# Optimization experiments

Measured on AMD Instinct MI355X. Metric: run time of the kernel, lower is better.

The kernel has to match this reference:

```python
import jax, jax.numpy as jnp
import numpy as np
import math

DIM = 1024
NUM_HEADS = 16
HEAD_DIM = 64
SEQ_LEN = 2048
ATTN_SCALE = 0.12


def cosine_norm(x, eps=1e-12):
    # unit-normalize along last dim
    return x * jax.lax.rsqrt(jnp.sum(x * x, axis=-1, keepdims=True) + eps)


def rotary_tables(T, head_dim):
    dim_quarter = max(1, head_dim // 4)
    angular_freq = (1.0 / 1024.0) ** jnp.linspace(0.0, 1.0, dim_quarter, dtype=jnp.float32)
    angular_freq = jnp.concatenate([angular_freq, jnp.zeros(dim_quarter, dtype=jnp.float32)])  # [head_dim//2]
    t = jnp.arange(T, dtype=jnp.float32)
    theta = t[:, None] * angular_freq[None, :]  # [T, head_dim//2]
    return jnp.cos(theta), jnp.sin(theta)


def apply_rotary(x_BTHD, cos, sin):
    # cos/sin: [T, head_dim//2] -> broadcast [1, T, 1, head_dim//2]
    c = cos[None, :, None, :]
    s = sin[None, :, None, :]
    x1, x2 = jnp.split(x_BTHD, 2, axis=-1)
    y1 = x1 * c + x2 * s
    y2 = -x1 * s + x2 * c
    return jnp.concatenate([y1, y2], axis=-1)


def setup_inputs() -> dict:
    key = jax.random.key(0)
    ks = jax.random.split(key, 6)
    x = jax.random.normal(ks[0], (1, SEQ_LEN, DIM), dtype=jnp.float32)
    init_std = 0.02
    Wq = jax.random.normal(ks[1], (DIM, NUM_HEADS * HEAD_DIM), dtype=jnp.float32) * init_std
    Wk = jax.random.normal(ks[2], (DIM, NUM_HEADS * HEAD_DIM), dtype=jnp.float32) * init_std
    Wv = jax.random.normal(ks[3], (DIM, NUM_HEADS * HEAD_DIM), dtype=jnp.float32) * init_std
    Wo = jax.random.normal(ks[4], (NUM_HEADS * HEAD_DIM, DIM), dtype=jnp.float32) * init_std
    # Scale param: initialized as ones * (1/sqrt(dim)); use rand around that magnitude
    s_qk = jax.random.uniform(ks[5], (NUM_HEADS, HEAD_DIM), dtype=jnp.float32,
                              minval=0.5, maxval=1.5) * (1.0 / math.sqrt(DIM))
    return {"x": x, "Wq": Wq, "Wk": Wk, "Wv": Wv, "Wo": Wo, "s_qk": s_qk}


def reference(x, Wq, Wk, Wv, Wo, s_qk):
    B, T, _ = x.shape
    # projections
    q = (x @ Wq).reshape(B, T, NUM_HEADS, HEAD_DIM)
    k = (x @ Wk).reshape(B, T, NUM_HEADS, HEAD_DIM)
    v = (x @ Wv).reshape(B, T, NUM_HEADS, HEAD_DIM)
    # effective scale: s * (init/scale) with init=1, scale=1/sqrt(dim)
    s_eff = s_qk * math.sqrt(DIM)  # [H, D]
    q = cosine_norm(q) * s_eff[None, None, :, :]
    k = cosine_norm(k) * s_eff[None, None, :, :]
    cos, sin = rotary_tables(T, HEAD_DIM)
    q = apply_rotary(q, cos, sin)
    k = apply_rotary(k, cos, sin)
    # causal attention with fixed scale 0.12 (block_mask == causal)
    scores = jnp.einsum('bthd,bshd->bhts', q, k) * ATTN_SCALE  # [B,H,T,T]
    causal = jnp.tril(jnp.ones((T, T), dtype=bool))
    scores = jnp.where(causal[None, None, :, :], scores, jnp.float32(-1e30))
    attn = jax.nn.softmax(scores, axis=-1)
    y = jnp.einsum('bhts,bshd->bthd', attn, v)
    y = y.reshape(B, T, NUM_HEADS * HEAD_DIM)
    return y @ Wo
```

## Files before the change

### kernel.cpp

```cpp
#include <hip/hip_runtime.h>

typedef unsigned short u16;
typedef unsigned int u32;
typedef __attribute__((ext_vector_type(8))) short bf16x8;
typedef __attribute__((ext_vector_type(4))) float f32x4;

__device__ __forceinline__ u16 f2bf(float x) {
  unsigned u = __float_as_uint(x);
  u += 0x7fffu + ((u >> 16) & 1u);
  return (u16)(u >> 16);
}
__device__ __forceinline__ float bf2f(u16 z) {
  return __uint_as_float((u32)z << 16);
}

__global__ __launch_bounds__(256) void cast_kernel(const float* __restrict__ in,
                                                   u16* __restrict__ out, int n,
                                                   float2* __restrict__ rtab) {
  int g = blockIdx.x * 256 + threadIdx.x;
  int i = g * 4;
  if (i < n) {
    float4 f = *(const float4*)(in + i);
    ushort4 o;
    o.x = f2bf(f.x); o.y = f2bf(f.y); o.z = f2bf(f.z); o.w = f2bf(f.w);
    *(ushort4*)(out + i) = o;
  }
  if (g < 2048 * 16) {
    int t = g >> 4, ii = g & 15;
    float fr = exp2f(-10.0f * (float)ii / 15.0f);
    float th = (float)t * fr;
    rtab[g] = make_float2(cosf(th), sinf(th));
  }
}

__global__ __launch_bounds__(256) void transcast(const float* __restrict__ W0,
                                                 const float* __restrict__ W1,
                                                 const float* __restrict__ W2,
                                                 const float* __restrict__ W3,
                                                 u16* __restrict__ out) {
  __shared__ alignas(16) u16 ls[64 * 72];
  int z = blockIdx.z;
  const float* W = (z == 0) ? W0 : (z == 1) ? W1 : (z == 2) ? W2 : W3;
  u16* o = out + (size_t)z * (1024u * 1024u);
  int kt = blockIdx.y * 64, nt = blockIdx.x * 64;
  int tid = threadIdx.x;
  int r = tid >> 2, c0 = (tid & 3) * 16;
  const float* src = W + (size_t)(kt + r) * 1024 + nt + c0;
  u16 tmp[16];
#pragma unroll
  for (int c = 0; c < 16; c += 4) {
    float4 f = *(const float4*)(src + c);
    tmp[c + 0] = f2bf(f.x); tmp[c + 1] = f2bf(f.y);
    tmp[c + 2] = f2bf(f.z); tmp[c + 3] = f2bf(f.w);
  }
#pragma unroll
  for (int c = 0; c < 16; ++c) ls[r * 72 + c0 + c] = tmp[c];
  __syncthreads();
#pragma unroll
  for (int pass = 0; pass < 4; ++pass) {
    int n = pass * 16 + (tid >> 4);
    int kk = (tid & 15) * 4;
    ushort4 val;
    val.x = ls[(kk + 0) * 72 + n];
    val.y = ls[(kk + 1) * 72 + n];
    val.z = ls[(kk + 2) * 72 + n];
    val.w = ls[(kk + 3) * 72 + n];
    *(ushort4*)(o + (size_t)(nt + n) * 1024 + kt + kk) = val;
  }
}

#define GLD 40

__global__ __launch_bounds__(256) void gemm_qkv(const u16* __restrict__ A,
                                                const u16* __restrict__ Wt,
                                                u16* __restrict__ qb,
                                                u16* __restrict__ kb,
                                                u16* __restrict__ vt,
                                                const float* __restrict__ s_qk,
                                                const float2* __restrict__ rtab) {
  __shared__ alignas(16) u16 As[128 * GLD];
  __shared__ alignas(16) u16 Bs[128 * GLD];
  int z = blockIdx.z;
  const u16* B = Wt + (size_t)z * (1024u * 1024u);
  int tid = threadIdx.x;
  int bm = blockIdx.y * 128, bn = blockIdx.x * 128;
  int lane = tid & 63, w = tid >> 6;
  int wm = (w >> 1) * 64, wn = (w & 1) * 64;
  int m16 = lane & 15, q = lane >> 4;
  f32x4 acc[4][4] = {};
  int srow = tid >> 1, scol = (tid & 1) * 16;
  const u16* aptr = A + (size_t)(bm + srow) * 1024 + scol;
  const u16* bptr = B + (size_t)(bn + srow) * 1024 + scol;
  uint4 a0 = *(const uint4*)(aptr);
  uint4 a1 = *(const uint4*)(aptr + 8);
  uint4 b0 = *(const uint4*)(bptr);
  uint4 b1 = *(const uint4*)(bptr + 8);
  for (int k0 = 0; k0 < 1024; k0 += 32) {
    __syncthreads();
    *(uint4*)&As[srow * GLD + scol] = a0;
    *(uint4*)&As[srow * GLD + scol + 8] = a1;
    *(uint4*)&Bs[srow * GLD + scol] = b0;
    *(uint4*)&Bs[srow * GLD + scol + 8] = b1;
    uint4 na0, na1, nb0, nb1;
    if (k0 < 992) {
      na0 = *(const uint4*)(aptr + k0 + 32);
      na1 = *(const uint4*)(aptr + k0 + 40);
      nb0 = *(const uint4*)(bptr + k0 + 32);
      nb1 = *(const uint4*)(bptr + k0 + 40);
    }
    __syncthreads();
    bf16x8 af[4], bfr[4];
#pragma unroll
    for (int mt = 0; mt < 4; ++mt)
      af[mt] = *(const bf16x8*)&As[(wm + mt * 16 + m16) * GLD + q * 8];
#pragma unroll
    for (int nt = 0; nt < 4; ++nt)
      bfr[nt] = *(const bf16x8*)&Bs[(wn + nt * 16 + m16) * GLD + q * 8];
#pragma unroll
    for (int mt = 0; mt < 4; ++mt)
#pragma unroll
      for (int nt = 0; nt < 4; ++nt)
        acc[mt][nt] = __builtin_amdgcn_mfma_f32_16x16x32_bf16(af[mt], bfr[nt], acc[mt][nt], 0, 0, 0);
    if (k0 < 992) { a0 = na0; a1 = na1; b0 = nb0; b1 = nb1; }
  }
  int hh = (bn + wn) >> 6;
  if (z == 2) {
#pragma unroll
    for (int nt = 0; nt < 4; ++nt) {
      int n = bn + wn + nt * 16 + m16;
#pragma unroll
      for (int mt = 0; mt < 4; ++mt) {
        int t0 = bm + wm + mt * 16 + q * 4;
        ushort4 val;
        val.x = f2bf(acc[mt][nt][0]);
        val.y = f2bf(acc[mt][nt][1]);
        val.z = f2bf(acc[mt][nt][2]);
        val.w = f2bf(acc[mt][nt][3]);
        *(ushort4*)(vt + (size_t)n * 2048 + t0) = val;
      }
    }
  } else {
    u16* dst = z ? kb : qb;
    float se0 = s_qk[hh * 64 +  0 + m16] * 32.0f;
    float se1 = s_qk[hh * 64 + 16 + m16] * 32.0f;
    float se2 = s_qk[hh * 64 + 32 + m16] * 32.0f;
    float se3 = s_qk[hh * 64 + 48 + m16] * 32.0f;
#pragma unroll
    for (int mt = 0; mt < 4; ++mt)
#pragma unroll
      for (int r = 0; r < 4; ++r) {
        float ss = acc[mt][0][r] * acc[mt][0][r] + acc[mt][1][r] * acc[mt][1][r]
                 + acc[mt][2][r] * acc[mt][2][r] + acc[mt][3][r] * acc[mt][3][r];
        ss += __shfl_xor(ss, 1); ss += __shfl_xor(ss, 2);
        ss += __shfl_xor(ss, 4); ss += __shfl_xor(ss, 8);
        float inv = rsqrtf(ss + 1e-12f);
        int t = bm + wm + mt * 16 + q * 4 + r;
        float2 cs = rtab[t * 16 + m16];
        float x0 = acc[mt][0][r] * inv * se0;
        float x1 = acc[mt][1][r] * inv * se1;
        float x2 = acc[mt][2][r] * inv * se2;
        float x3 = acc[mt][3][r] * inv * se3;
        size_t off = (size_t)t * 1024 + hh * 64 + m16;
        dst[off]      = f2bf(x0 * cs.x + x2 * cs.y);
        dst[off + 16] = f2bf(x1);
        dst[off + 32] = f2bf(x2 * cs.x - x0 * cs.y);
        dst[off + 48] = f2bf(x3);
      }
  }
}

#define ALD 72
__global__ __launch_bounds__(256) void attn_fold(const u16* __restrict__ qb,
                                                 const u16* __restrict__ kb,
                                                 const u16* __restrict__ vt,
                                                 u16* __restrict__ yb) {
  __shared__ alignas(16) u16 Ks[64 * ALD];
  __shared__ alignas(16) u16 Vt[64 * ALD];
  __shared__ alignas(16) u16 Ps[4 * 16 * ALD];
  int h = blockIdx.x;
  int y = blockIdx.y;
  int tid = threadIdx.x;
  int lane = tid & 63, w = tid >> 6;
  int m16 = lane & 15, q = lane >> 4;
  int krow_s = tid >> 2, kcol_s = (tid & 3) * 16;
  const u16* kbase = kb + (size_t)krow_s * 1024 + h * 64 + kcol_s;
  const u16* vbase = vt + (size_t)(h * 64 + krow_s) * 2048 + kcol_s;
  u16* pw = &Ps[w * 16 * ALD];
#pragma unroll 1
  for (int half = 0; half < 2; ++half) {
    int qt = half ? y : 31 - y;
    int t0 = qt * 64;
    const u16* qrow = qb + (size_t)(t0 + w * 16 + m16) * 1024 + h * 64;
    bf16x8 qa0 = *(const bf16x8*)(qrow + q * 8);
    bf16x8 qa1 = *(const bf16x8*)(qrow + 32 + q * 8);
    f32x4 Yacc[4] = {};
    float lsum[4] = {0.f, 0.f, 0.f, 0.f};
    int trow = t0 + w * 16 + q * 4;
    uint4 kv0 = *(const uint4*)kbase;
    uint4 kv1 = *(const uint4*)(kbase + 8);
    uint4 vv0 = *(const uint4*)vbase;
    uint4 vv1 = *(const uint4*)(vbase + 8);
    for (int jt = 0; jt <= qt; ++jt) {
      __syncthreads();
      *(uint4*)&Ks[krow_s * ALD + kcol_s] = kv0;
      *(uint4*)&Ks[krow_s * ALD + kcol_s + 8] = kv1;
      *(uint4*)&Vt[krow_s * ALD + kcol_s] = vv0;
      *(uint4*)&Vt[krow_s * ALD + kcol_s + 8] = vv1;
      uint4 kn0, kn1, vn0, vn1;
      if (jt < qt) {
        const u16* kp = kbase + (size_t)(jt + 1) * 65536;
        const u16* vp = vbase + (jt + 1) * 64;
        kn0 = *(const uint4*)kp;
        kn1 = *(const uint4*)(kp + 8);
        vn0 = *(const uint4*)vp;
        vn1 = *(const uint4*)(vp + 8);
      }
      __syncthreads();
      f32x4 S[4] = {};
#pragma unroll
      for (int nt = 0; nt < 4; ++nt) {
        bf16x8 b0 = *(const bf16x8*)&Ks[(nt * 16 + m16) * ALD + q * 8];
        bf16x8 b1 = *(const bf16x8*)&Ks[(nt * 16 + m16) * ALD + 32 + q * 8];
        S[nt] = __builtin_amdgcn_mfma_f32_16x16x32_bf16(qa0, b0, S[nt], 0, 0, 0);
        S[nt] = __builtin_amdgcn_mfma_f32_16x16x32_bf16(qa1, b1, S[nt], 0, 0, 0);
      }
      bool diag = (jt == qt);
      int j0 = jt * 64;
      float tmp[4] = {0.f, 0.f, 0.f, 0.f};
#pragma unroll
      for (int nt = 0; nt < 4; ++nt) {
        int j = j0 + nt * 16 + m16;
#pragma unroll
        for (int r = 0; r < 4; ++r) {
          float p = __builtin_amdgcn_exp2f(S[nt][r] * 0.17312340490667562f);
          if (diag && (j > trow + r)) p = 0.f;
          tmp[r] += p;
          pw[(q * 4 + r) * ALD + nt * 16 + m16] = f2bf(p);
        }
      }
#pragma unroll
      for (int r = 0; r < 4; ++r) {
        float s = tmp[r];
        s += __shfl_xor(s, 1); s += __shfl_xor(s, 2);
        s += __shfl_xor(s, 4); s += __shfl_xor(s, 8);
        lsum[r] += s;
      }
      bf16x8 pa0 = *(const bf16x8*)&pw[m16 * ALD + q * 8];
      bf16x8 pa1 = *(const bf16x8*)&pw[m16 * ALD + 32 + q * 8];
#pragma unroll
      for (int nt = 0; nt < 4; ++nt) {
        bf16x8 b0 = *(const bf16x8*)&Vt[(nt * 16 + m16) * ALD + q * 8];
        bf16x8 b1 = *(const bf16x8*)&Vt[(nt * 16 + m16) * ALD + 32 + q * 8];
        Yacc[nt] = __builtin_amdgcn_mfma_f32_16x16x32_bf16(pa0, b0, Yacc[nt], 0, 0, 0);
        Yacc[nt] = __builtin_amdgcn_mfma_f32_16x16x32_bf16(pa1, b1, Yacc[nt], 0, 0, 0);
      }
      if (jt < qt) { kv0 = kn0; kv1 = kn1; vv0 = vn0; vv1 = vn1; }
    }
#pragma unroll
    for (int r = 0; r < 4; ++r) {
      float inv = __builtin_amdgcn_rcpf(lsum[r]);
      int t = t0 + w * 16 + q * 4 + r;
#pragma unroll
      for (int nt = 0; nt < 4; ++nt)
        yb[(size_t)t * 1024 + h * 64 + nt * 16 + m16] = f2bf(Yacc[nt][r] * inv);
    }
  }
}

__global__ __launch_bounds__(256) void gemm_o(const u16* __restrict__ A,
                                              const u16* __restrict__ B,
                                              float* __restrict__ C) {
  __shared__ alignas(16) u16 As[128 * GLD];
  __shared__ alignas(16) u16 Bs[64 * GLD];
  int tid = threadIdx.x;
  int bm = blockIdx.y * 128, bn = blockIdx.x * 64;
  int lane = tid & 63, w = tid >> 6;
  int wm = w * 32;
  int m16 = lane & 15, q = lane >> 4;
  f32x4 acc[2][4] = {};
  int srA = tid >> 1, scA = (tid & 1) * 16;
  int srB = tid >> 2, scB = (tid & 3) * 8;
  const u16* aptr = A + (size_t)(bm + srA) * 1024 + scA;
  const u16* bptr = B + (size_t)(bn + srB) * 1024 + scB;
  uint4 a0 = *(const uint4*)(aptr);
  uint4 a1 = *(const uint4*)(aptr + 8);
  uint4 b0 = *(const uint4*)(bptr);
  for (int k0 = 0; k0 < 1024; k0 += 32) {
    __syncthreads();
    *(uint4*)&As[srA * GLD + scA] = a0;
    *(uint4*)&As[srA * GLD + scA + 8] = a1;
    *(uint4*)&Bs[srB * GLD + scB] = b0;
    uint4 na0, na1, nb0;
    if (k0 < 992) {
      na0 = *(const uint4*)(aptr + k0 + 32);
      na1 = *(const uint4*)(aptr + k0 + 40);
      nb0 = *(const uint4*)(bptr + k0 + 32);
    }
    __syncthreads();
    bf16x8 af[2], bfr[4];
#pragma unroll
    for (int mt = 0; mt < 2; ++mt)
      af[mt] = *(const bf16x8*)&As[(wm + mt * 16 + m16) * GLD + q * 8];
#pragma unroll
    for (int nt = 0; nt < 4; ++nt)
      bfr[nt] = *(const bf16x8*)&Bs[(nt * 16 + m16) * GLD + q * 8];
#pragma unroll
    for (int mt = 0; mt < 2; ++mt)
#pragma unroll
      for (int nt = 0; nt < 4; ++nt)
        acc[mt][nt] = __builtin_amdgcn_mfma_f32_16x16x32_bf16(af[mt], bfr[nt], acc[mt][nt], 0, 0, 0);
    if (k0 < 992) { a0 = na0; a1 = na1; b0 = nb0; }
  }
#pragma unroll
  for (int mt = 0; mt < 2; ++mt)
#pragma unroll
    for (int nt = 0; nt < 4; ++nt)
#pragma unroll
      for (int r = 0; r < 4; ++r) {
        int row = bm + wm + mt * 16 + q * 4 + r;
        int col = bn + nt * 16 + m16;
        C[(size_t)row * 1024 + col] = acc[mt][nt][r];
      }
}

extern "C" void kernel_launch(void* const* d_in, const int* in_sizes, int n_in,
                              void* d_out, int out_size, void* d_ws, size_t ws_size,
                              hipStream_t stream) {
  const float* x   = (const float*)d_in[0];
  const float* Wq  = (const float*)d_in[1];
  const float* Wk  = (const float*)d_in[2];
  const float* Wv  = (const float*)d_in[3];
  const float* Wo  = (const float*)d_in[4];
  const float* sqk = (const float*)d_in[5];
  float* out = (float*)d_out;
  char* ws = (char*)d_ws;

  u16*    xb   = (u16*)ws;
  u16*    Wt   = (u16*)(ws + ((size_t)4 << 20));
  float2* rtab = (float2*)(ws + ((size_t)12 << 20));
  u16*    qb16 = (u16*)(ws + ((size_t)16 << 20));
  u16*    kb16 = (u16*)(ws + ((size_t)20 << 20));
  u16*    vt16 = (u16*)(ws + ((size_t)24 << 20));
  u16*    yb   = (u16*)(ws + ((size_t)28 << 20));
  u16*    Wto  = Wt + (size_t)3 * 1024 * 1024;

  cast_kernel<<<2048, 256, 0, stream>>>(x, xb, 2048 * 1024, rtab);
  transcast<<<dim3(16, 16, 4), 256, 0, stream>>>(Wq, Wk, Wv, Wo, Wt);
  gemm_qkv<<<dim3(8, 16, 3), 256, 0, stream>>>(xb, Wt, qb16, kb16, vt16, sqk, rtab);
  attn_fold<<<dim3(16, 16), 256, 0, stream>>>(qb16, kb16, vt16, yb);
  gemm_o<<<dim3(16, 16), 256, 0, stream>>>(yb, Wto, out);
}
```

Before: 153.5 us.

## Merge prep kernels and give each attention block one query tile

The x cast, rotary table setup and weight transpose-cast kernels are merged into one prep launch that picks its job from the block index, removing one kernel launch. The attention kernel stops folding two query tiles (qt and 31-qt) into one block and launches 16x32 blocks, each handling a single query tile, with longer-causal tiles scheduled first. This doubles the block count to fill more compute units, at the cost of uneven per-block work that the balanced folding used to smooth out.

```diff
diff --git a/kernel.cpp b/kernel.cpp
--- a/kernel.cpp
+++ b/kernel.cpp
@@ -14,36 +14,38 @@
   return __uint_as_float((u32)z << 16);
 }
 
-__global__ __launch_bounds__(256) void cast_kernel(const float* __restrict__ in,
-                                                   u16* __restrict__ out, int n,
-                                                   float2* __restrict__ rtab) {
-  int g = blockIdx.x * 256 + threadIdx.x;
-  int i = g * 4;
-  if (i < n) {
-    float4 f = *(const float4*)(in + i);
+__global__ __launch_bounds__(256) void prep(const float* __restrict__ x,
+                                            const float* __restrict__ W0,
+                                            const float* __restrict__ W1,
+                                            const float* __restrict__ W2,
+                                            const float* __restrict__ W3,
+                                            u16* __restrict__ xb,
+                                            u16* __restrict__ Wt,
+                                            float2* __restrict__ rtab) {
+  __shared__ alignas(16) u16 ls[64 * 72];
+  int b = blockIdx.x;
+  int tid = threadIdx.x;
+  if (b < 2048) {
+    int g = b * 256 + tid;
+    int i = g * 4;
+    float4 f = *(const float4*)(x + i);
     ushort4 o;
     o.x = f2bf(f.x); o.y = f2bf(f.y); o.z = f2bf(f.z); o.w = f2bf(f.w);
-    *(ushort4*)(out + i) = o;
-  }
-  if (g < 2048 * 16) {
-    int t = g >> 4, ii = g & 15;
-    float fr = exp2f(-10.0f * (float)ii / 15.0f);
-    float th = (float)t * fr;
-    rtab[g] = make_float2(cosf(th), sinf(th));
-  }
-}
-
-__global__ __launch_bounds__(256) void transcast(const float* __restrict__ W0,
-                                                 const float* __restrict__ W1,
-                                                 const float* __restrict__ W2,
-                                                 const float* __restrict__ W3,
-                                                 u16* __restrict__ out) {
-  __shared__ alignas(16) u16 ls[64 * 72];
-  int z = blockIdx.z;
+    *(ushort4*)(xb + i) = o;
+    if (g < 2048 * 16) {
+      int t = g >> 4, ii = g & 15;
+      float fr = exp2f(-10.0f * (float)ii / 15.0f);
+      float th = (float)t * fr;
+      rtab[g] = make_float2(cosf(th), sinf(th));
+    }
+    return;
+  }
+  int bb = b - 2048;
+  int z = bb >> 8;
+  int rem = bb & 255;
   const float* W = (z == 0) ? W0 : (z == 1) ? W1 : (z == 2) ? W2 : W3;
-  u16* o = out + (size_t)z * (1024u * 1024u);
-  int kt = blockIdx.y * 64, nt = blockIdx.x * 64;
-  int tid = threadIdx.x;
+  u16* o = Wt + (size_t)z * (1024u * 1024u);
+  int kt = (rem >> 4) * 64, nt = (rem & 15) * 64;
   int r = tid >> 2, c0 = (tid & 3) * 16;
   const float* src = W + (size_t)(kt + r) * 1024 + nt + c0;
   u16 tmp[16];
@@ -170,15 +172,16 @@
 }
 
 #define ALD 72
-__global__ __launch_bounds__(256) void attn_fold(const u16* __restrict__ qb,
-                                                 const u16* __restrict__ kb,
-                                                 const u16* __restrict__ vt,
-                                                 u16* __restrict__ yb) {
+__global__ __launch_bounds__(256) void attn_flash(const u16* __restrict__ qb,
+                                                  const u16* __restrict__ kb,
+                                                  const u16* __restrict__ vt,
+                                                  u16* __restrict__ yb) {
   __shared__ alignas(16) u16 Ks[64 * ALD];
   __shared__ alignas(16) u16 Vt[64 * ALD];
   __shared__ alignas(16) u16 Ps[4 * 16 * ALD];
   int h = blockIdx.x;
-  int y = blockIdx.y;
+  int qt = 31 - blockIdx.y;
+  int t0 = qt * 64;
   int tid = threadIdx.x;
   int lane = tid & 63, w = tid >> 6;
   int m16 = lane & 15, q = lane >> 4;
@@ -186,84 +189,79 @@
   const u16* kbase = kb + (size_t)krow_s * 1024 + h * 64 + kcol_s;
   const u16* vbase = vt + (size_t)(h * 64 + krow_s) * 2048 + kcol_s;
   u16* pw = &Ps[w * 16 * ALD];
-#pragma unroll 1
-  for (int half = 0; half < 2; ++half) {
-    int qt = half ? y : 31 - y;
-    int t0 = qt * 64;
-    const u16* qrow = qb + (size_t)(t0 + w * 16 + m16) * 1024 + h * 64;
-    bf16x8 qa0 = *(const bf16x8*)(qrow + q * 8);
-    bf16x8 qa1 = *(const bf16x8*)(qrow + 32 + q * 8);
-    f32x4 Yacc[4] = {};
-    float lsum[4] = {0.f, 0.f, 0.f, 0.f};
-    int trow = t0 + w * 16 + q * 4;
-    uint4 kv0 = *(const uint4*)kbase;
-    uint4 kv1 = *(const uint4*)(kbase + 8);
-    uint4 vv0 = *(const uint4*)vbase;
-    uint4 vv1 = *(const uint4*)(vbase + 8);
-    for (int jt = 0; jt <= qt; ++jt) {
-      __syncthreads();
-      *(uint4*)&Ks[krow_s * ALD + kcol_s] = kv0;
-      *(uint4*)&Ks[krow_s * ALD + kcol_s + 8] = kv1;
-      *(uint4*)&Vt[krow_s * ALD + kcol_s] = vv0;
-      *(uint4*)&Vt[krow_s * ALD + kcol_s + 8] = vv1;
-      uint4 kn0, kn1, vn0, vn1;
-      if (jt < qt) {
-        const u16* kp = kbase + (size_t)(jt + 1) * 65536;
-        const u16* vp = vbase + (jt + 1) * 64;
-        kn0 = *(const uint4*)kp;
-        kn1 = *(const uint4*)(kp + 8);
-        vn0 = *(const uint4*)vp;
-        vn1 = *(const uint4*)(vp + 8);
+  const u16* qrow = qb + (size_t)(t0 + w * 16 + m16) * 1024 + h * 64;
+  bf16x8 qa0 = *(const bf16x8*)(qrow + q * 8);
+  bf16x8 qa1 = *(const bf16x8*)(qrow + 32 + q * 8);
+  f32x4 Yacc[4] = {};
+  float lsum[4] = {0.f, 0.f, 0.f, 0.f};
+  int trow = t0 + w * 16 + q * 4;
+  uint4 kv0 = *(const uint4*)kbase;
+  uint4 kv1 = *(const uint4*)(kbase + 8);
+  uint4 vv0 = *(const uint4*)vbase;
+  uint4 vv1 = *(const uint4*)(vbase + 8);
+  for (int jt = 0; jt <= qt; ++jt) {
+    __syncthreads();
+    *(uint4*)&Ks[krow_s * ALD + kcol_s] = kv0;
+    *(uint4*)&Ks[krow_s * ALD + kcol_s + 8] = kv1;
+    *(uint4*)&Vt[krow_s * ALD + kcol_s] = vv0;
+    *(uint4*)&Vt[krow_s * ALD + kcol_s + 8] = vv1;
+    uint4 kn0, kn1, vn0, vn1;
+    if (jt < qt) {
+      const u16* kp = kbase + (size_t)(jt + 1) * 65536;
+      const u16* vp = vbase + (jt + 1) * 64;
+      kn0 = *(const uint4*)kp;
+      kn1 = *(const uint4*)(kp + 8);
+      vn0 = *(const uint4*)vp;
+      vn1 = *(const uint4*)(vp + 8);
+    }
+    __syncthreads();
+    f32x4 S[4] = {};
+#pragma unroll
+    for (int nt = 0; nt < 4; ++nt) {
+      bf16x8 b0 = *(const bf16x8*)&Ks[(nt * 16 + m16) * ALD + q * 8];
+      bf16x8 b1 = *(const bf16x8*)&Ks[(nt * 16 + m16) * ALD + 32 + q * 8];
+      S[nt] = __builtin_amdgcn_mfma_f32_16x16x32_bf16(qa0, b0, S[nt], 0, 0, 0);
+      S[nt] = __builtin_amdgcn_mfma_f32_16x16x32_bf16(qa1, b1, S[nt], 0, 0, 0);
+    }
+    bool diag = (jt == qt);
+    int j0 = jt * 64;
+    float tmp[4] = {0.f, 0.f, 0.f, 0.f};
+#pragma unroll
+    for (int nt = 0; nt < 4; ++nt) {
+      int j = j0 + nt * 16 + m16;
+#pragma unroll
+      for (int r = 0; r < 4; ++r) {
+        float p = __builtin_amdgcn_exp2f(S[nt][r] * 0.17312340490667562f);
+        if (diag && (j > trow + r)) p = 0.f;
+        tmp[r] += p;
+        pw[(q * 4 + r) * ALD + nt * 16 + m16] = f2bf(p);
       }
-      __syncthreads();
-      f32x4 S[4] = {};
-#pragma unroll
-      for (int nt = 0; nt < 4; ++nt) {
-        bf16x8 b0 = *(const bf16x8*)&Ks[(nt * 16 + m16) * ALD + q * 8];
-        bf16x8 b1 = *(const bf16x8*)&Ks[(nt * 16 + m16) * ALD + 32 + q * 8];
-        S[nt] = __builtin_amdgcn_mfma_f32_16x16x32_bf16(qa0, b0, S[nt], 0, 0, 0);
-        S[nt] = __builtin_amdgcn_mfma_f32_16x16x32_bf16(qa1, b1, S[nt], 0, 0, 0);
-      }
-      bool diag = (jt == qt);
-      int j0 = jt * 64;
-      float tmp[4] = {0.f, 0.f, 0.f, 0.f};
-#pragma unroll
-      for (int nt = 0; nt < 4; ++nt) {
-        int j = j0 + nt * 16 + m16;
-#pragma unroll
-        for (int r = 0; r < 4; ++r) {
-          float p = __builtin_amdgcn_exp2f(S[nt][r] * 0.17312340490667562f);
-          if (diag && (j > trow + r)) p = 0.f;
-          tmp[r] += p;
-          pw[(q * 4 + r) * ALD + nt * 16 + m16] = f2bf(p);
-        }
-      }
-#pragma unroll
-      for (int r = 0; r < 4; ++r) {
-        float s = tmp[r];
-        s += __shfl_xor(s, 1); s += __shfl_xor(s, 2);
-        s += __shfl_xor(s, 4); s += __shfl_xor(s, 8);
-        lsum[r] += s;
-      }
-      bf16x8 pa0 = *(const bf16x8*)&pw[m16 * ALD + q * 8];
-      bf16x8 pa1 = *(const bf16x8*)&pw[m16 * ALD + 32 + q * 8];
-#pragma unroll
-      for (int nt = 0; nt < 4; ++nt) {
-        bf16x8 b0 = *(const bf16x8*)&Vt[(nt * 16 + m16) * ALD + q * 8];
-        bf16x8 b1 = *(const bf16x8*)&Vt[(nt * 16 + m16) * ALD + 32 + q * 8];
-        Yacc[nt] = __builtin_amdgcn_mfma_f32_16x16x32_bf16(pa0, b0, Yacc[nt], 0, 0, 0);
-        Yacc[nt] = __builtin_amdgcn_mfma_f32_16x16x32_bf16(pa1, b1, Yacc[nt], 0, 0, 0);
-      }
-      if (jt < qt) { kv0 = kn0; kv1 = kn1; vv0 = vn0; vv1 = vn1; }
     }
 #pragma unroll
     for (int r = 0; r < 4; ++r) {
-      float inv = __builtin_amdgcn_rcpf(lsum[r]);
-      int t = t0 + w * 16 + q * 4 + r;
-#pragma unroll
-      for (int nt = 0; nt < 4; ++nt)
-        yb[(size_t)t * 1024 + h * 64 + nt * 16 + m16] = f2bf(Yacc[nt][r] * inv);
-    }
+      float s = tmp[r];
+      s += __shfl_xor(s, 1); s += __shfl_xor(s, 2);
+      s += __shfl_xor(s, 4); s += __shfl_xor(s, 8);
+      lsum[r] += s;
+    }
+    bf16x8 pa0 = *(const bf16x8*)&pw[m16 * ALD + q * 8];
+    bf16x8 pa1 = *(const bf16x8*)&pw[m16 * ALD + 32 + q * 8];
+#pragma unroll
+    for (int nt = 0; nt < 4; ++nt) {
+      bf16x8 b0 = *(const bf16x8*)&Vt[(nt * 16 + m16) * ALD + q * 8];
+      bf16x8 b1 = *(const bf16x8*)&Vt[(nt * 16 + m16) * ALD + 32 + q * 8];
+      Yacc[nt] = __builtin_amdgcn_mfma_f32_16x16x32_bf16(pa0, b0, Yacc[nt], 0, 0, 0);
+      Yacc[nt] = __builtin_amdgcn_mfma_f32_16x16x32_bf16(pa1, b1, Yacc[nt], 0, 0, 0);
+    }
+    if (jt < qt) { kv0 = kn0; kv1 = kn1; vv0 = vn0; vv1 = vn1; }
+  }
+#pragma unroll
+  for (int r = 0; r < 4; ++r) {
+    float inv = __builtin_amdgcn_rcpf(lsum[r]);
+    int t = t0 + w * 16 + q * 4 + r;
+#pragma unroll
+    for (int nt = 0; nt < 4; ++nt)
+      yb[(size_t)t * 1024 + h * 64 + nt * 16 + m16] = f2bf(Yacc[nt][r] * inv);
   }
 }
 
@@ -344,9 +342,8 @@
   u16*    yb   = (u16*)(ws + ((size_t)28 << 20));
   u16*    Wto  = Wt + (size_t)3 * 1024 * 1024;
 
-  cast_kernel<<<2048, 256, 0, stream>>>(x, xb, 2048 * 1024, rtab);
-  transcast<<<dim3(16, 16, 4), 256, 0, stream>>>(Wq, Wk, Wv, Wo, Wt);
+  prep<<<3072, 256, 0, stream>>>(x, Wq, Wk, Wv, Wo, xb, Wt, rtab);
   gemm_qkv<<<dim3(8, 16, 3), 256, 0, stream>>>(xb, Wt, qb16, kb16, vt16, sqk, rtab);
-  attn_fold<<<dim3(16, 16), 256, 0, stream>>>(qb16, kb16, vt16, yb);
+  attn_flash<<<dim3(16, 32), 256, 0, stream>>>(qb16, kb16, vt16, yb);
   gemm_o<<<dim3(16, 16), 256, 0, stream>>>(yb, Wto, out);
 }
```

Result: no change. 154.0 us (+0.3%).
